# Kernel optimization log

Hardware: AMD Instinct MI355X
Metric: run time of the kernel (lower is better)

Reference implementation:

```python
import jax, jax.numpy as jnp
import numpy as np

N_STATE = 512
M_IN = 64
P_OUT = 64
BATCH = 32
SEQ = 2048


def setup_inputs() -> dict:
    key = jax.random.key(0)
    k1, k2, k3, k4, k5 = jax.random.split(key, 5)
    u = jax.random.normal(k1, (BATCH, SEQ, M_IN), dtype=jnp.float32)
    # CompanionParam init: a ~ randn * 0.01 (keeps companion matrix stable, near shift matrix)
    a = jax.random.normal(k2, (N_STATE,), dtype=jnp.float32) * 0.01
    B = jax.random.normal(k3, (N_STATE, M_IN), dtype=jnp.float32) * 0.05
    C = jax.random.normal(k4, (P_OUT, N_STATE), dtype=jnp.float32) * 0.05
    D = jax.random.normal(k5, (P_OUT, M_IN), dtype=jnp.float32) * 0.05
    return {"u": u, "a": a, "B": B, "C": C, "D": D}


def companion_matrix(a):
    # A[i+1, i] = 1 on subdiagonal; last column = -flip(a)  (matches CompanionParam.matrix)
    n = a.shape[0]
    idx = jnp.arange(n - 1)
    A = jnp.zeros((n, n), dtype=a.dtype)
    A = A.at[idx + 1, idx].set(1.0)
    A = A.at[:, n - 1].set(-a[::-1])
    return A


def reference(u, a, B, C, D):
    # LTI SSM recurrence: x_t = A x_{t-1} + B u_t ; y_t = C x_t + D u_t
    A = companion_matrix(a)  # (n, n)
    batch, T, m = u.shape
    n = a.shape[0]
    u_t = jnp.transpose(u, (1, 0, 2))  # (T, batch, m)
    Bu = jnp.einsum('tbm,nm->tbn', u_t, B)  # precompute input drive (T, batch, n)

    def step(x, bu):
        x_new = x @ A.T + bu  # (batch, n)
        return x_new, x_new

    x0 = jnp.zeros((batch, n), dtype=u.dtype)
    _, xs = jax.lax.scan(step, x0, Bu)  # xs: (T, batch, n)
    ys = jnp.einsum('tbn,pn->tbp', xs, C) + jnp.einsum('tbm,pm->tbp', u_t, D)
    return jnp.transpose(ys, (1, 0, 2))  # (batch, T, p)
```

## Files before the change

### kernel.cpp

```cpp
#include <hip/hip_runtime.h>

#define SEQ  2048
#define NB   32
#define NS   512
#define MI   64
#define PO   64
#define TB   64
#define NTB  32
#define CH   64
#define NCH  8
#define LDU  72
#define LDD  68
#define SG_LDA 72

typedef __attribute__((ext_vector_type(8))) __bf16 bf16x8;
typedef __attribute__((ext_vector_type(4))) float  floatx4;

__device__ inline unsigned short f2bf(float f) {
    unsigned u = __builtin_bit_cast(unsigned, f);
    u += 0x7fff + ((u >> 16) & 1);
    return (unsigned short)(u >> 16);
}

__global__ void __launch_bounds__(256) prep_all_kernel(
    const float* __restrict__ u, const float* __restrict__ B,
    const float* __restrict__ C, const float* __restrict__ D,
    const float* __restrict__ a,
    unsigned short* __restrict__ ubf, unsigned short* __restrict__ BflatT,
    unsigned short* __restrict__ Bws, unsigned short* __restrict__ Cws,
    unsigned short* __restrict__ Dws, unsigned short* __restrict__ qT) {
    __shared__ float a_ext[1024];
    const int bx = blockIdx.x, tid = threadIdx.x;
    if (bx < 2048) {
        const size_t base = ((size_t)bx * 256 + tid) * 8;
        float4 f0 = *(const float4*)(u + base);
        float4 f1 = *(const float4*)(u + base + 4);
        unsigned short tmp[8];
        tmp[0] = f2bf(f0.x); tmp[1] = f2bf(f0.y); tmp[2] = f2bf(f0.z); tmp[3] = f2bf(f0.w);
        tmp[4] = f2bf(f1.x); tmp[5] = f2bf(f1.y); tmp[6] = f2bf(f1.z); tmp[7] = f2bf(f1.w);
        *(uint4*)(ubf + base) = *(uint4*)&tmp[0];
    } else if (bx < 2560) {
        const int i = bx - 2048;
        for (int r = 0; r < 2; ++r) {
            const int id = tid + r * 256;
            const int j = id >> 3, q8 = (id & 7) * 8;
            unsigned short tmp[8];
            if (i >= j) {
                const float4 f0 = *(const float4*)(B + (size_t)(i - j) * MI + q8);
                const float4 f1 = *(const float4*)(B + (size_t)(i - j) * MI + q8 + 4);
                tmp[0] = f2bf(f0.x); tmp[1] = f2bf(f0.y); tmp[2] = f2bf(f0.z); tmp[3] = f2bf(f0.w);
                tmp[4] = f2bf(f1.x); tmp[5] = f2bf(f1.y); tmp[6] = f2bf(f1.z); tmp[7] = f2bf(f1.w);
            } else {
#pragma unroll
                for (int z = 0; z < 8; ++z) tmp[z] = 0;
            }
            *(uint4*)(BflatT + (size_t)i * 4096 + j * 64 + q8) = *(uint4*)&tmp[0];
        }
    } else if (bx < 2624) {
        const int p = bx - 2560;
        for (int x = tid; x < 1024; x += 256) a_ext[x] = (x < NS) ? a[x] : 0.f;
        __syncthreads();
        const int j0 = tid, j1 = tid + 256;
        float acc0 = 0.f, acc1 = 0.f;
        const float4* crow = (const float4*)(C + (size_t)p * NS);
        for (int i4 = 0; i4 < NS / 4; ++i4) {
            const float4 cv = crow[i4];
            const int base = 511 - i4 * 4;
            acc0 += cv.x * a_ext[base + j0]     + cv.y * a_ext[base - 1 + j0] +
                    cv.z * a_ext[base - 2 + j0] + cv.w * a_ext[base - 3 + j0];
            acc1 += cv.x * a_ext[base + j1]     + cv.y * a_ext[base - 1 + j1] +
                    cv.z * a_ext[base - 2 + j1] + cv.w * a_ext[base - 3 + j1];
        }
        qT[(size_t)p * NS + j0] = f2bf(acc0);
        qT[(size_t)p * NS + j1] = f2bf(acc1);
    } else {
        const int idx = (bx - 2624) * 256 + tid;
        const int nB = NS * MI, nC = PO * NS, nD = PO * MI;
        if (idx < nB) Bws[idx] = f2bf(B[idx]);
        else if (idx < nB + nC) Cws[idx - nB] = f2bf(C[idx - nB]);
        else if (idx < nB + nC + nD) Dws[idx - nB - nC] = f2bf(D[idx - nB - nC]);
    }
}

__global__ void __launch_bounds__(256) sgemm_kernel(const unsigned short* __restrict__ ubf,
                                                    const unsigned short* __restrict__ BflatT,
                                                    float* __restrict__ Sbuf) {
    __shared__ unsigned short A_l[4 * 64 * SG_LDA];
    __shared__ unsigned short U_l[4 * 32 * SG_LDA];
    const int ib = blockIdx.x, b = blockIdx.y;
    const int tid = threadIdx.x, lane = tid & 63, w = tid >> 6;
    const int row16 = lane & 15, quad = lane >> 4;
    const int i0 = ib * 64;
    floatx4 acc[2];
#pragma unroll
    for (int ns = 0; ns < 2; ++ns) acc[ns] = (floatx4){0.f, 0.f, 0.f, 0.f};

    for (int jg = 0; jg < 16; ++jg) {
#pragma unroll
        for (int r = 0; r < 8; ++r) {
            const int id = tid + r * 256;
            const int row = id >> 5;
            const int jj = (id >> 3) & 3, q8 = (id & 7) * 8;
            const int j = jg * 4 + jj;
            *(uint4*)&A_l[(jj * 64 + row) * SG_LDA + q8] =
                *(const uint4*)(BflatT + (size_t)(i0 + row) * 4096 + j * 64 + q8);
        }
#pragma unroll
        for (int r = 0; r < 4; ++r) {
            const int id = tid + r * 256;
            const int n = id >> 5;
            const int jj = (id >> 3) & 3, q8 = (id & 7) * 8;
            const int j = jg * 4 + jj;
            *(uint4*)&U_l[(jj * 32 + n) * SG_LDA + q8] =
                *(const uint4*)(ubf + ((size_t)b * SEQ + n * 64 + 63 - j) * MI + q8);
        }
        __syncthreads();
#pragma unroll
        for (int jj = 0; jj < 4; ++jj) {
#pragma unroll
            for (int mk = 0; mk < 2; ++mk) {
                const bf16x8 av = *(const bf16x8*)
                    &A_l[(jj * 64 + w * 16 + row16) * SG_LDA + mk * 32 + quad * 8];
#pragma unroll
                for (int ns = 0; ns < 2; ++ns) {
                    const bf16x8 bv = *(const bf16x8*)
                        &U_l[(jj * 32 + ns * 16 + row16) * SG_LDA + mk * 32 + quad * 8];
                    acc[ns] = __builtin_amdgcn_mfma_f32_16x16x32_bf16(av, bv, acc[ns], 0, 0, 0);
                }
            }
        }
        __syncthreads();
    }
#pragma unroll
    for (int ns = 0; ns < 2; ++ns) {
        const int n = ns * 16 + row16;
        float* dst = Sbuf + ((size_t)b * NTB + n) * NS + i0 + w * 16 + quad * 4;
        *(floatx4*)dst = acc[ns];
    }
}

__global__ void __launch_bounds__(1024) scan_himp_kernel(const float* __restrict__ Sbuf,
                                                         float* __restrict__ Rbuf,
                                                         const float* __restrict__ a,
                                                         float* __restrict__ hbuf) {
    __shared__ __align__(16) char smem[24576];
    const int tid = threadIdx.x;
    if (blockIdx.x < NB) {
        const int b = blockIdx.x;
        const float4* S4 = (const float4*)(Sbuf + (size_t)b * NTB * NS);
        float4* R4 = (float4*)(Rbuf + (size_t)b * NTB * NS);
        for (int o = tid; o < NTB * NS / 4; o += 1024) {
            const int k = o >> 7;
            const int i4 = o & 127;
            float4 acc = make_float4(0.f, 0.f, 0.f, 0.f);
#pragma unroll
            for (int m = 0; m < 8; ++m) {
                if (m <= k - 1 && i4 >= 16 * m) {
                    const float4 s = S4[(k - 1 - m) * 128 + i4 - 16 * m];
                    acc.x += s.x; acc.y += s.y; acc.z += s.z; acc.w += s.w;
                }
            }
            R4[o] = acc;
        }
    } else {
        float* a_l     = (float*)smem;
        float* h_ext   = (float*)(smem + 2560);
        float* part    = (float*)(smem + 12800);
        float* rhs_ext = (float*)(smem + 20992);
        const int kk = tid & 63, grp = tid >> 6;

        for (int x = tid; x < 640; x += 1024) a_l[x] = (x < NS) ? a[x] : 0.f;
        for (int x = tid; x < 640; x += 1024) h_ext[x] = 0.f;
        if (tid < 256) rhs_ext[tid] = 0.f;
        __syncthreads();

        float aw[34];
#pragma unroll
        for (int i = 0; i < 34; ++i) aw[i] = a_l[2 * kk + grp * 32 + i];

        if (tid < 64) {
            if (tid == 0) h_ext[512] = 1.f;
            float acc = (tid >= 1) ? a_l[tid - 1] : 0.f;
            for (int s = 1; s < 64; ++s) {
                const float hs = -__shfl(acc, s);
                if (tid == s) h_ext[512 + s] = hs;
                const float av = a_l[(tid > s) ? (tid - 1 - s) : 0];
                acc += (tid > s) ? av * hs : 0.f;
            }
        }
        __syncthreads();

        int t0 = 64;
        while (t0 < SEQ) {
            float acc0 = 0.f, acc1 = 0.f;
#pragma unroll
            for (int m = 0; m < 8; ++m) {
                const float4 hv = *(const float4*)&h_ext[512 + t0 - grp * 32 - 4 - 4 * m];
                acc0 += aw[4 * m + 0] * hv.w + aw[4 * m + 1] * hv.z +
                        aw[4 * m + 2] * hv.y + aw[4 * m + 3] * hv.x;
                acc1 += aw[4 * m + 1] * hv.w + aw[4 * m + 2] * hv.z +
                        aw[4 * m + 3] * hv.y + aw[4 * m + 4] * hv.x;
            }
            *(float2*)&part[grp * 128 + 2 * kk] = make_float2(acc0, acc1);
            __syncthreads();
            if (tid < 128) {
                float r = 0.f;
#pragma unroll
                for (int g = 0; g < 16; ++g) r += part[g * 128 + tid];
                rhs_ext[128 + tid] = -r;
            }
            __syncthreads();
            {
                const int g = tid >> 7, out = tid & 127;
                const int k0 = g * 16;
                float s = 0.f;
#pragma unroll
                for (int k4 = 0; k4 < 4; ++k4) {
                    const float4 h4 = *(const float4*)&h_ext[512 + k0 + 4 * k4];
                    const int base = 128 + out - k0 - 4 * k4;
                    s += h4.x * rhs_ext[base]     + h4.y * rhs_ext[base - 1] +
                         h4.z * rhs_ext[base - 2] + h4.w * rhs_ext[base - 3];
                }
                part[g * 128 + out] = s;
            }
            __syncthreads();
            if (tid < 128) {
                float r = 0.f;
#pragma unroll
                for (int g = 0; g < 8; ++g) r += part[g * 128 + tid];
                h_ext[512 + t0 + tid] = r;
            }
            __syncthreads();
            t0 += (t0 == 64) ? 64 : 128;
        }
        for (int i = tid; i < SEQ; i += 1024) hbuf[i] = h_ext[512 + i];
    }
}

__global__ void __launch_bounds__(256, 4) ytile_kernel(
    const unsigned short* __restrict__ ubf, const unsigned short* __restrict__ Bws,
    const unsigned short* __restrict__ Cws, const unsigned short* __restrict__ Dws,
    const float* __restrict__ Rbuf, float* __restrict__ fbuf, float* __restrict__ y) {
    __shared__ unsigned short u_b[TB * LDU];
    __shared__ float buDiag[TB * LDD];
    __shared__ unsigned short Gb[TB * LDU];
    __shared__ float sgrp[4][TB];
    __shared__ float psplitL[TB];
    __shared__ float exitBuf[2][TB];

    const int blk = blockIdx.x, b = blockIdx.y;
    const int t0 = blk * TB;
    const int tid = threadIdx.x;
    const int lane = tid & 63, w = tid >> 6;
    const int row16 = lane & 15, quad = lane >> 4;
    const int dsc = lane;
    const int g = w;
    const size_t rbase = ((size_t)b * NTB + blk) * NS;
    const int tsplit = 63 - dsc, gsplit = tsplit >> 4, jsplit = tsplit & 15;

    float sA = (dsc >= 1) ? Rbuf[rbase + dsc - 1] : 0.f;

#pragma unroll
    for (int r = 0; r < 2; ++r) {
        const int id = tid + r * 256;
        const int t = id >> 3, q8 = (id & 7) * 8;
        *(uint4*)&u_b[t * LDU + q8] =
            *(const uint4*)(ubf + ((size_t)b * SEQ + t0 + t) * MI + q8);
    }

    floatx4 accY[4];
#pragma unroll
    for (int nt = 0; nt < 4; ++nt) accY[nt] = (floatx4){0.f, 0.f, 0.f, 0.f};
    __syncthreads();

    bf16x8 ufr0[4], ufr1[4];
#pragma unroll
    for (int nt = 0; nt < 4; ++nt) {
        const int t = nt * 16 + row16;
        ufr0[nt] = *(const bf16x8*)&u_b[t * LDU + quad * 8];
        ufr1[nt] = *(const bf16x8*)&u_b[t * LDU + 32 + quad * 8];
    }

    int cur = 0;
    for (int ch = 0; ch < NCH; ++ch) {
        float sA_next = 0.f;
        if (ch + 1 < NCH) sA_next = Rbuf[rbase + (ch + 1) * 64 + dsc - 1];

        const bf16x8 bf0 = *(const bf16x8*)(Bws + (size_t)(ch * CH + w * 16 + row16) * MI + quad * 8);
        const bf16x8 bf1 = *(const bf16x8*)(Bws + (size_t)(ch * CH + w * 16 + row16) * MI + 32 + quad * 8);
        const bf16x8 cf0 = *(const bf16x8*)(Cws + (size_t)(w * 16 + row16) * NS + ch * CH + quad * 8);
        const bf16x8 cf1 = *(const bf16x8*)(Cws + (size_t)(w * 16 + row16) * NS + ch * CH + 32 + quad * 8);

#pragma unroll
        for (int nt = 0; nt < 4; ++nt) {
            floatx4 dacc = {0.f, 0.f, 0.f, 0.f};
            dacc = __builtin_amdgcn_mfma_f32_16x16x32_bf16(bf0, ufr0[nt], dacc, 0, 0, 0);
            dacc = __builtin_amdgcn_mfma_f32_16x16x32_bf16(bf1, ufr1[nt], dacc, 0, 0, 0);
            const int t = nt * 16 + row16;
            const int ibase = w * 16 + quad * 4;
#pragma unroll
            for (int r = 0; r < 4; ++r) {
                const int dd = (ibase + r - t) & 63;
                buDiag[dd * LDD + t] = dacc[r];
            }
        }
        __syncthreads();

        float pv[16];
        {
            const float* row = &buDiag[dsc * LDD + g * 16];
            const float4 v0 = *(const float4*)(row + 0);
            const float4 v1 = *(const float4*)(row + 4);
            const float4 v2 = *(const float4*)(row + 8);
            const float4 v3 = *(const float4*)(row + 12);
            pv[0]  = v0.x;          pv[1]  = pv[0]  + v0.y;
            pv[2]  = pv[1]  + v0.z; pv[3]  = pv[2]  + v0.w;
            pv[4]  = pv[3]  + v1.x; pv[5]  = pv[4]  + v1.y;
            pv[6]  = pv[5]  + v1.z; pv[7]  = pv[6]  + v1.w;
            pv[8]  = pv[7]  + v2.x; pv[9]  = pv[8]  + v2.y;
            pv[10] = pv[9]  + v2.z; pv[11] = pv[10] + v2.w;
            pv[12] = pv[11] + v3.x; pv[13] = pv[12] + v3.y;
            pv[14] = pv[13] + v3.z; pv[15] = pv[14] + v3.w;
        }
        sgrp[g][dsc] = pv[15];
        __syncthreads();

        const float s0 = sgrp[0][dsc], s1 = sgrp[1][dsc], s2 = sgrp[2][dsc];
        const float off = (g > 0 ? s0 : 0.f) + (g > 1 ? s1 : 0.f) + (g > 2 ? s2 : 0.f);
        float plocal = pv[0];
#pragma unroll
        for (int j = 1; j < 16; ++j) plocal = (j == jsplit) ? pv[j] : plocal;
        if (g == gsplit) {
            const float Ps = off + plocal;
            psplitL[dsc] = Ps;
            const float ev = sA + Ps;
            if (ch == NCH - 1) fbuf[(size_t)b * SEQ + t0 + tsplit] = ev;
            else exitBuf[cur ^ 1][dsc] = ev;
        }
        __syncthreads();

        {
            const float Ps = psplitL[dsc];
            const float cB = (ch > 0) ? exitBuf[cur][dsc] : 0.f;
#pragma unroll
            for (int j = 0; j < 16; ++j) {
                const int t = g * 16 + j;
                const float incl = off + pv[j];
                const float out = (t <= tsplit) ? (sA + incl) : (cB + (incl - Ps));
                Gb[t * LDU + ((dsc + t) & 63)] = f2bf(out);
            }
        }
        __syncthreads();

#pragma unroll
        for (int nt = 0; nt < 4; ++nt) {
            const int t = nt * 16 + row16;
            bf16x8 g0 = *(const bf16x8*)&Gb[t * LDU + quad * 8];
            bf16x8 g1 = *(const bf16x8*)&Gb[t * LDU + 32 + quad * 8];
            accY[nt] = __builtin_amdgcn_mfma_f32_16x16x32_bf16(cf0, g0, accY[nt], 0, 0, 0);
            accY[nt] = __builtin_amdgcn_mfma_f32_16x16x32_bf16(cf1, g1, accY[nt], 0, 0, 0);
        }
        sA = sA_next;
        cur ^= 1;
    }

    const bf16x8 df0 = *(const bf16x8*)(Dws + (size_t)(w * 16 + row16) * MI + quad * 8);
    const bf16x8 df1 = *(const bf16x8*)(Dws + (size_t)(w * 16 + row16) * MI + 32 + quad * 8);
#pragma unroll
    for (int nt = 0; nt < 4; ++nt) {
        const int t = nt * 16 + row16;
        accY[nt] = __builtin_amdgcn_mfma_f32_16x16x32_bf16(df0, ufr0[nt], accY[nt], 0, 0, 0);
        accY[nt] = __builtin_amdgcn_mfma_f32_16x16x32_bf16(df1, ufr1[nt], accY[nt], 0, 0, 0);
        const int p0 = w * 16 + quad * 4;
        *(floatx4*)(y + ((size_t)b * SEQ + t0 + t) * PO + p0) = accY[nt];
    }
}

__global__ void __launch_bounds__(256) sconv_kernel(const float* __restrict__ fbuf,
                                                    const float* __restrict__ hbuf,
                                                    float* __restrict__ sbuf) {
    __shared__ float f_l[SEQ];
    __shared__ float h_lc[SEQ + 8];
    __shared__ float part[4][TB];
    const int blk = blockIdx.x, b = blockIdx.y, tid = threadIdx.x;
    const int t0 = blk * TB;
    const int len = t0 + TB;
    {
        const float4* fs = (const float4*)(fbuf + (size_t)b * SEQ);
        const float4* hs = (const float4*)hbuf;
        for (int i = tid; i < len / 4; i += 256) {
            ((float4*)f_l)[i] = fs[i];
            ((float4*)h_lc)[i] = hs[i];
        }
    }
    __syncthreads();
    const int dt = tid & 63, grp = tid >> 6;
    const int t = t0 + dt;
    float acc = 0.f;
    for (int j4 = grp * 4; j4 <= t; j4 += 16) {
        const float4 hv = *(const float4*)&h_lc[j4];
        if (j4 + 0 <= t) acc += hv.x * f_l[t - j4 - 0];
        if (j4 + 1 <= t) acc += hv.y * f_l[t - j4 - 1];
        if (j4 + 2 <= t) acc += hv.z * f_l[t - j4 - 2];
        if (j4 + 3 <= t) acc += hv.w * f_l[t - j4 - 3];
    }
    part[grp][dt] = acc;
    __syncthreads();
    if (tid < TB) {
        sbuf[(size_t)b * SEQ + t0 + tid] =
            part[0][tid] + part[1][tid] + part[2][tid] + part[3][tid];
    }
}

__global__ void __launch_bounds__(256) corr_kernel(
    const float* __restrict__ sbuf, const unsigned short* __restrict__ qT,
    float* __restrict__ y) {
    __shared__ float s_l[NS + TB];
    __shared__ unsigned short Sw[2][TB * LDU];
    const int blk = blockIdx.x, b = blockIdx.y, tid = threadIdx.x;
    const int t0 = blk * TB;
    const int lane = tid & 63, w = tid >> 6;
    const int row16 = lane & 15, quad = lane >> 4;
    for (int idx = tid; idx < NS + TB; idx += 256) {
        const int t = t0 - NS + idx;
        s_l[idx] = (t >= 0) ? sbuf[(size_t)b * SEQ + t] : 0.f;
    }
    floatx4 acc[4];
#pragma unroll
    for (int nt = 0; nt < 4; ++nt) acc[nt] = (floatx4){0.f, 0.f, 0.f, 0.f};
    __syncthreads();

    for (int ch = 0; ch < NCH; ++ch) {
        const int buf = ch & 1;
        const bf16x8 qf0 = *(const bf16x8*)(qT + (size_t)(w * 16 + row16) * NS + ch * CH + quad * 8);
        const bf16x8 qf1 = *(const bf16x8*)(qT + (size_t)(w * 16 + row16) * NS + ch * CH + 32 + quad * 8);
        {
            const int r = tid >> 2, c0 = (tid & 3) * 16;
            unsigned short tmp[16];
            const int base = 511 + r - ch * CH - c0;
#pragma unroll
            for (int jj = 0; jj < 16; ++jj) tmp[jj] = f2bf(s_l[base - jj]);
            *(uint4*)&Sw[buf][r * LDU + c0]     = *(uint4*)&tmp[0];
            *(uint4*)&Sw[buf][r * LDU + c0 + 8] = *(uint4*)&tmp[8];
        }
        __syncthreads();
#pragma unroll
        for (int nt = 0; nt < 4; ++nt) {
            const int t = nt * 16 + row16;
            bf16x8 s0 = *(const bf16x8*)&Sw[buf][t * LDU + quad * 8];
            bf16x8 s1 = *(const bf16x8*)&Sw[buf][t * LDU + 32 + quad * 8];
            acc[nt] = __builtin_amdgcn_mfma_f32_16x16x32_bf16(qf0, s0, acc[nt], 0, 0, 0);
            acc[nt] = __builtin_amdgcn_mfma_f32_16x16x32_bf16(qf1, s1, acc[nt], 0, 0, 0);
        }
    }
#pragma unroll
    for (int nt = 0; nt < 4; ++nt) {
        const int t = nt * 16 + row16;
        const int p0 = w * 16 + quad * 4;
        float* yp = y + ((size_t)b * SEQ + t0 + t) * PO + p0;
        floatx4 old = *(const floatx4*)yp;
        *(floatx4*)yp = old - acc[nt];
    }
}

extern "C" void kernel_launch(void* const* d_in, const int* in_sizes, int n_in,
                              void* d_out, int out_size, void* d_ws,
                              size_t ws_size, hipStream_t stream) {
    const float* u  = (const float*)d_in[0];
    const float* a  = (const float*)d_in[1];
    const float* B  = (const float*)d_in[2];
    const float* Cm = (const float*)d_in[3];
    const float* Dm = (const float*)d_in[4];
    float* y = (float*)d_out;

    char* ws = (char*)d_ws;
    unsigned short* Bws = (unsigned short*)ws;                  ws += NS * MI * 2;
    unsigned short* Cws = (unsigned short*)ws;                  ws += PO * NS * 2;
    unsigned short* Dws = (unsigned short*)ws;                  ws += PO * MI * 2;
    unsigned short* qTw = (unsigned short*)ws;                  ws += PO * NS * 2;
    unsigned short* ubf = (unsigned short*)ws;                  ws += (size_t)NB * SEQ * MI * 2;
    unsigned short* Bft = (unsigned short*)ws;                  ws += (size_t)NS * 4096 * 2;
    float* Sbuf = (float*)ws;                                   ws += (size_t)NB * NTB * NS * 4;
    float* Rbuf = (float*)ws;                                   ws += (size_t)NB * NTB * NS * 4;
    float* fbuf = (float*)ws;                                   ws += (size_t)NB * SEQ * 4;
    float* sbuf = (float*)ws;                                   ws += (size_t)NB * SEQ * 4;
    float* hbuf = (float*)ws;

    prep_all_kernel<<<dim3(2896), dim3(256), 0, stream>>>(
        u, B, Cm, Dm, a, ubf, Bft, Bws, Cws, Dws, qTw);
    sgemm_kernel<<<dim3(8, 32), dim3(256), 0, stream>>>(ubf, Bft, Sbuf);
    scan_himp_kernel<<<dim3(NB + 1), dim3(1024), 0, stream>>>(Sbuf, Rbuf, a, hbuf);
    ytile_kernel<<<dim3(NTB, NB), dim3(256), 0, stream>>>(
        ubf, Bws, Cws, Dws, Rbuf, fbuf, y);
    sconv_kernel<<<dim3(NTB, NB), dim3(256), 0, stream>>>(fbuf, hbuf, sbuf);
    corr_kernel<<<dim3(NTB, NB), dim3(256), 0, stream>>>(sbuf, qTw, y);
}
```

Measured before the change: 220.4 us.

## Use wavefront shuffles for diagonal prefix scan and register-block the causal convolution

The ytile kernel remaps threads so that each wave owns 16 diagonals, with 4 lanes per diagonal. Cross-segment offsets and the split value now come from __shfl instead of shared-memory staging, which removes two block barriers per chunk plus the sgrp, psplitL and exitBuf arrays. The carry from the previous chunk stays in a register, and u fragments load straight from global memory rather than through LDS. The sconv kernel now has each thread compute 4 consecutive outputs from zero-padded float4 windows, which cuts the per-element branches and LDS loads at the cost of a 16-way partial reduction.

```diff
diff --git a/kernel.cpp b/kernel.cpp
--- a/kernel.cpp
+++ b/kernel.cpp
@@ -241,50 +241,39 @@
     const unsigned short* __restrict__ ubf, const unsigned short* __restrict__ Bws,
     const unsigned short* __restrict__ Cws, const unsigned short* __restrict__ Dws,
     const float* __restrict__ Rbuf, float* __restrict__ fbuf, float* __restrict__ y) {
-    __shared__ unsigned short u_b[TB * LDU];
-    __shared__ float buDiag[TB * LDD];
-    __shared__ unsigned short Gb[TB * LDU];
-    __shared__ float sgrp[4][TB];
-    __shared__ float psplitL[TB];
-    __shared__ float exitBuf[2][TB];
+    __shared__ __align__(16) float buDiag[TB * LDD];
+    __shared__ __align__(16) unsigned short Gb[TB * LDU];
 
     const int blk = blockIdx.x, b = blockIdx.y;
     const int t0 = blk * TB;
     const int tid = threadIdx.x;
     const int lane = tid & 63, w = tid >> 6;
     const int row16 = lane & 15, quad = lane >> 4;
-    const int dsc = lane;
-    const int g = w;
     const size_t rbase = ((size_t)b * NTB + blk) * NS;
-    const int tsplit = 63 - dsc, gsplit = tsplit >> 4, jsplit = tsplit & 15;
-
-    float sA = (dsc >= 1) ? Rbuf[rbase + dsc - 1] : 0.f;
-
-#pragma unroll
-    for (int r = 0; r < 2; ++r) {
-        const int id = tid + r * 256;
-        const int t = id >> 3, q8 = (id & 7) * 8;
-        *(uint4*)&u_b[t * LDU + q8] =
-            *(const uint4*)(ubf + ((size_t)b * SEQ + t0 + t) * MI + q8);
-    }
+
+    const int dd = lane >> 2, seg = lane & 3;
+    const int d  = w * 16 + dd;
+    const int tsplit = 63 - d, gseg = tsplit >> 4, jsplit = tsplit & 15;
+    const int qb = lane & 60;
+
+    float sA = (d >= 1) ? Rbuf[rbase + d - 1] : 0.f;
+    float cB = 0.f;
 
     floatx4 accY[4];
 #pragma unroll
     for (int nt = 0; nt < 4; ++nt) accY[nt] = (floatx4){0.f, 0.f, 0.f, 0.f};
-    __syncthreads();
 
     bf16x8 ufr0[4], ufr1[4];
 #pragma unroll
     for (int nt = 0; nt < 4; ++nt) {
-        const int t = nt * 16 + row16;
-        ufr0[nt] = *(const bf16x8*)&u_b[t * LDU + quad * 8];
-        ufr1[nt] = *(const bf16x8*)&u_b[t * LDU + 32 + quad * 8];
-    }
-
-    int cur = 0;
+        const size_t ub = ((size_t)b * SEQ + t0 + nt * 16 + row16) * MI;
+        ufr0[nt] = *(const bf16x8*)(ubf + ub + quad * 8);
+        ufr1[nt] = *(const bf16x8*)(ubf + ub + 32 + quad * 8);
+    }
+
     for (int ch = 0; ch < NCH; ++ch) {
         float sA_next = 0.f;
-        if (ch + 1 < NCH) sA_next = Rbuf[rbase + (ch + 1) * 64 + dsc - 1];
+        if (ch + 1 < NCH) sA_next = Rbuf[rbase + (ch + 1) * 64 + d - 1];
 
         const bf16x8 bf0 = *(const bf16x8*)(Bws + (size_t)(ch * CH + w * 16 + row16) * MI + quad * 8);
         const bf16x8 bf1 = *(const bf16x8*)(Bws + (size_t)(ch * CH + w * 16 + row16) * MI + 32 + quad * 8);
@@ -300,19 +289,19 @@
             const int ibase = w * 16 + quad * 4;
 #pragma unroll
             for (int r = 0; r < 4; ++r) {
-                const int dd = (ibase + r - t) & 63;
-                buDiag[dd * LDD + t] = dacc[r];
-            }
-        }
-        __syncthreads();
-
-        float pv[16];
+                const int dscat = (ibase + r - t) & 63;
+                buDiag[dscat * LDD + t] = dacc[r];
+            }
+        }
+        __syncthreads();
+
         {
-            const float* row = &buDiag[dsc * LDD + g * 16];
-            const float4 v0 = *(const float4*)(row + 0);
-            const float4 v1 = *(const float4*)(row + 4);
-            const float4 v2 = *(const float4*)(row + 8);
-            const float4 v3 = *(const float4*)(row + 12);
+            const float* rowp = &buDiag[d * LDD + seg * 16];
+            const float4 v0 = *(const float4*)(rowp + 0);
+            const float4 v1 = *(const float4*)(rowp + 4);
+            const float4 v2 = *(const float4*)(rowp + 8);
+            const float4 v3 = *(const float4*)(rowp + 12);
+            float pv[16];
             pv[0]  = v0.x;          pv[1]  = pv[0]  + v0.y;
             pv[2]  = pv[1]  + v0.z; pv[3]  = pv[2]  + v0.w;
             pv[4]  = pv[3]  + v1.x; pv[5]  = pv[4]  + v1.y;
@@ -321,34 +310,29 @@
             pv[10] = pv[9]  + v2.z; pv[11] = pv[10] + v2.w;
             pv[12] = pv[11] + v3.x; pv[13] = pv[12] + v3.y;
             pv[14] = pv[13] + v3.z; pv[15] = pv[14] + v3.w;
-        }
-        sgrp[g][dsc] = pv[15];
-        __syncthreads();
-
-        const float s0 = sgrp[0][dsc], s1 = sgrp[1][dsc], s2 = sgrp[2][dsc];
-        const float off = (g > 0 ? s0 : 0.f) + (g > 1 ? s1 : 0.f) + (g > 2 ? s2 : 0.f);
-        float plocal = pv[0];
-#pragma unroll
-        for (int j = 1; j < 16; ++j) plocal = (j == jsplit) ? pv[j] : plocal;
-        if (g == gsplit) {
-            const float Ps = off + plocal;
-            psplitL[dsc] = Ps;
-            const float ev = sA + Ps;
-            if (ch == NCH - 1) fbuf[(size_t)b * SEQ + t0 + tsplit] = ev;
-            else exitBuf[cur ^ 1][dsc] = ev;
-        }
-        __syncthreads();
-
-        {
-            const float Ps = psplitL[dsc];
-            const float cB = (ch > 0) ? exitBuf[cur][dsc] : 0.f;
+            const float total = pv[15];
+            const float tq0 = __shfl(total, qb + 0);
+            const float tq1 = __shfl(total, qb + 1);
+            const float tq2 = __shfl(total, qb + 2);
+            const float off = (seg > 0 ? tq0 : 0.f) + (seg > 1 ? tq1 : 0.f) +
+                              (seg > 2 ? tq2 : 0.f);
+            float plocal = pv[0];
+#pragma unroll
+            for (int j = 1; j < 16; ++j) plocal = (j == jsplit) ? pv[j] : plocal;
+            const float Ps = __shfl(off + plocal, qb + gseg);
+            const float exitv = sA + Ps;
+            const float baseLo = sA, baseHi = cB - Ps;
 #pragma unroll
             for (int j = 0; j < 16; ++j) {
-                const int t = g * 16 + j;
-                const float incl = off + pv[j];
-                const float out = (t <= tsplit) ? (sA + incl) : (cB + (incl - Ps));
-                Gb[t * LDU + ((dsc + t) & 63)] = f2bf(out);
-            }
+                const int t = seg * 16 + j;
+                const float outv = ((t <= tsplit) ? baseLo : baseHi) + off + pv[j];
+                Gb[t * LDU + ((d + t) & 63)] = f2bf(outv);
+            }
+            if (ch == NCH - 1) {
+                if (seg == 0) fbuf[(size_t)b * SEQ + t0 + tsplit] = exitv;
+            }
+            cB = exitv;
+            sA = sA_next;
         }
         __syncthreads();
 
@@ -360,8 +344,6 @@
             accY[nt] = __builtin_amdgcn_mfma_f32_16x16x32_bf16(cf0, g0, accY[nt], 0, 0, 0);
             accY[nt] = __builtin_amdgcn_mfma_f32_16x16x32_bf16(cf1, g1, accY[nt], 0, 0, 0);
         }
-        sA = sA_next;
-        cur ^= 1;
     }
 
     const bf16x8 df0 = *(const bf16x8*)(Dws + (size_t)(w * 16 + row16) * MI + quad * 8);
@@ -379,36 +361,44 @@
 __global__ void __launch_bounds__(256) sconv_kernel(const float* __restrict__ fbuf,
                                                     const float* __restrict__ hbuf,
                                                     float* __restrict__ sbuf) {
-    __shared__ float f_l[SEQ];
-    __shared__ float h_lc[SEQ + 8];
-    __shared__ float part[4][TB];
+    __shared__ __align__(16) float f_l[64 + SEQ];
+    __shared__ __align__(16) float h_lc[SEQ + 8];
+    __shared__ __align__(16) float part[16][TB];
     const int blk = blockIdx.x, b = blockIdx.y, tid = threadIdx.x;
     const int t0 = blk * TB;
     const int len = t0 + TB;
     {
         const float4* fs = (const float4*)(fbuf + (size_t)b * SEQ);
         const float4* hs = (const float4*)hbuf;
-        for (int i = tid; i < len / 4; i += 256) {
-            ((float4*)f_l)[i] = fs[i];
-            ((float4*)h_lc)[i] = hs[i];
-        }
+        float4* f4 = (float4*)f_l;
+        float4* h4p = (float4*)h_lc;
+        if (tid < 16) f4[tid] = make_float4(0.f, 0.f, 0.f, 0.f);
+        for (int i = tid; i < len / 4; i += 256) f4[16 + i] = fs[i];
+        const int nh4 = len / 4 + 2;
+        for (int i = tid; i < nh4; i += 256)
+            h4p[i] = (i < SEQ / 4) ? hs[i] : make_float4(0.f, 0.f, 0.f, 0.f);
     }
     __syncthreads();
-    const int dt = tid & 63, grp = tid >> 6;
-    const int t = t0 + dt;
-    float acc = 0.f;
-    for (int j4 = grp * 4; j4 <= t; j4 += 16) {
+    const int o4 = (tid & 15) * 4, grp = tid >> 4;
+    const int tb4 = t0 + o4;
+    float a0 = 0.f, a1 = 0.f, a2 = 0.f, a3 = 0.f;
+    for (int j4 = grp * 4; j4 <= tb4 + 3; j4 += 64) {
         const float4 hv = *(const float4*)&h_lc[j4];
-        if (j4 + 0 <= t) acc += hv.x * f_l[t - j4 - 0];
-        if (j4 + 1 <= t) acc += hv.y * f_l[t - j4 - 1];
-        if (j4 + 2 <= t) acc += hv.z * f_l[t - j4 - 2];
-        if (j4 + 3 <= t) acc += hv.w * f_l[t - j4 - 3];
-    }
-    part[grp][dt] = acc;
+        const int A = tb4 - j4;
+        const float4 q0 = *(const float4*)&f_l[60 + A];
+        const float4 q1 = *(const float4*)&f_l[64 + A];
+        a0 += hv.x * q1.x + hv.y * q0.w + hv.z * q0.z + hv.w * q0.y;
+        a1 += hv.x * q1.y + hv.y * q1.x + hv.z * q0.w + hv.w * q0.z;
+        a2 += hv.x * q1.z + hv.y * q1.y + hv.z * q1.x + hv.w * q0.w;
+        a3 += hv.x * q1.w + hv.y * q1.z + hv.z * q1.y + hv.w * q1.x;
+    }
+    *(float4*)&part[grp][o4] = make_float4(a0, a1, a2, a3);
     __syncthreads();
     if (tid < TB) {
-        sbuf[(size_t)b * SEQ + t0 + tid] =
-            part[0][tid] + part[1][tid] + part[2][tid] + part[3][tid];
+        float r = 0.f;
+#pragma unroll
+        for (int g = 0; g < 16; ++g) r += part[g][tid];
+        sbuf[(size_t)b * SEQ + t0 + tid] = r;
     }
 }
 
```

After: 204.0 us. -7.5%, faster.
